# Optimization experiments

Hardware: AMD Instinct MI355X
Metric: run time of the kernel (lower is better)

The kernel has to match this reference:

```python
import jax, jax.numpy as jnp
import numpy as np

B, T, L = 64, 1024, 400
E, D, A, K = 512, 80, 512, 5  # enc_odim, dec_odim, attn_dim, num mixture components


def setup_inputs() -> dict:
    key = jax.random.key(0)
    ks = jax.random.split(key, 24)
    g = lambda k, shape, fan: jax.random.normal(k, shape, jnp.float32) / np.sqrt(fan)
    return {
        "enc_z": jax.random.normal(ks[0], (B, T, E), jnp.float32),
        "ys": jax.random.normal(ks[1], (B, L, D), jnp.float32),
        "pre_W1": g(ks[2], (D, D), D), "pre_b1": jnp.zeros((D,), jnp.float32),
        "pre_W2": g(ks[3], (D, D), D), "pre_b2": jnp.zeros((D,), jnp.float32),
        # MOL attention GRU cell: input D -> hidden A (gates r,z,n)
        "gru_Wx": g(ks[4], (D, 3 * A), D), "gru_Wh": g(ks[5], (A, 3 * A), A),
        "gru_bx": jnp.zeros((3 * A,), jnp.float32), "gru_bh": jnp.zeros((3 * A,), jnp.float32),
        # MOL param net: Linear(A,A) + tanh + Linear(A, 3K)
        "att_W1": g(ks[6], (A, A), A), "att_b1": jnp.zeros((A,), jnp.float32),
        "att_W2": g(ks[7], (A, 3 * K), A), "att_b2": jnp.zeros((3 * K,), jnp.float32),
        # 2-layer LSTM: layer1 input E+A -> D, layer2 D -> D (gates i,f,g,o)
        "lstm_Wx1": g(ks[8], (E + A, 4 * D), E + A), "lstm_Wh1": g(ks[9], (D, 4 * D), D),
        "lstm_b1": jnp.zeros((4 * D,), jnp.float32),
        "lstm_Wx2": g(ks[10], (D, 4 * D), D), "lstm_Wh2": g(ks[11], (D, 4 * D), D),
        "lstm_b2": jnp.zeros((4 * D,), jnp.float32),
        # stop token projection
        "stop_W": g(ks[12], (D, 1), D), "stop_b": jnp.zeros((1,), jnp.float32),
    }


def _gru_cell(x, h, Wx, Wh, bx, bh):
    gx = x @ Wx + bx
    gh = h @ Wh + bh
    xr, xz, xn = jnp.split(gx, 3, axis=-1)
    hr, hz, hn = jnp.split(gh, 3, axis=-1)
    r = jax.nn.sigmoid(xr + hr)
    z = jax.nn.sigmoid(xz + hz)
    n = jnp.tanh(xn + r * hn)
    return (1.0 - z) * n + z * h


def _lstm_cell(x, h, c, Wx, Wh, b):
    gates = x @ Wx + h @ Wh + b
    i, f, g_, o = jnp.split(gates, 4, axis=-1)
    c_new = jax.nn.sigmoid(f) * c + jax.nn.sigmoid(i) * jnp.tanh(g_)
    h_new = jax.nn.sigmoid(o) * jnp.tanh(c_new)
    return h_new, c_new


def reference(enc_z, ys, pre_W1, pre_b1, pre_W2, pre_b2,
              gru_Wx, gru_Wh, gru_bx, gru_bh,
              att_W1, att_b1, att_W2, att_b2,
              lstm_Wx1, lstm_Wh1, lstm_b1, lstm_Wx2, lstm_Wh2, lstm_b2,
              stop_W, stop_b):
    b, t, e = enc_z.shape
    n_steps = ys.shape[1]
    d = pre_W1.shape[0]
    a = gru_Wh.shape[0]
    k = att_W2.shape[1] // 3
    pos = jnp.arange(t, dtype=jnp.float32)  # encoder positions

    def step(carry, _):
        h_att, means, h1, c1, h2, c2, prev_out = carry
        # prenet (eval mode)
        p = jax.nn.relu(prev_out @ pre_W1 + pre_b1)
        p = jax.nn.relu(p @ pre_W2 + pre_b2)
        # MOL attention: update attention RNN state, predict mixture params
        h_att = _gru_cell(p, h_att, gru_Wx, gru_Wh, gru_bx, gru_bh)
        params = jnp.tanh(h_att @ att_W1 + att_b1) @ att_W2 + att_b2  # [B, 3K]
        mu_hat, s_hat, w_hat = jnp.split(params, 3, axis=-1)
        means = means + jax.nn.softplus(mu_hat)            # monotonic means [B, K]
        scales = jax.nn.softplus(s_hat) + 1e-4             # [B, K]
        mix_w = jax.nn.softmax(w_hat, axis=-1)             # [B, K]
        # attention weights via logistic CDF differences: [B, T, K] -> [B, T]
        z_hi = (pos[None, :, None] + 0.5 - means[:, None, :]) / scales[:, None, :]
        z_lo = (pos[None, :, None] - 0.5 - means[:, None, :]) / scales[:, None, :]
        attn_w = jnp.einsum('btk,bk->bt', jax.nn.sigmoid(z_hi) - jax.nn.sigmoid(z_lo), mix_w)
        context = jnp.einsum('bt,bte->be', attn_w, enc_z)  # [B, E]
        # 2-layer LSTM
        x = jnp.concatenate([context, h_att], axis=-1)     # [B, E+A]
        h1, c1 = _lstm_cell(x, h1, c1, lstm_Wx1, lstm_Wh1, lstm_b1)
        h2, c2 = _lstm_cell(h1, h2, c2, lstm_Wx2, lstm_Wh2, lstm_b2)
        logit = (h2 @ stop_W + stop_b)[:, 0]               # [B]
        new_carry = (h_att, means, h1, c1, h2, c2, h2)     # feedback = decoder output
        return new_carry, (h2, logit)

    zf = lambda *s: jnp.zeros(s, jnp.float32)
    carry0 = (zf(b, a), zf(b, k), zf(b, d), zf(b, d), zf(b, d), zf(b, d), zf(b, d))
    _, (outs, logits) = jax.lax.scan(step, carry0, xs=None, length=n_steps)
    before = jnp.transpose(outs, (1, 0, 2))   # [B, L, D]
    after = before                             # postnet not applied inside loop
    return after, before, jnp.transpose(logits, (1, 0))  # [B, L]
```

## Files before the change

### kernel.cpp

```cpp
#include <hip/hip_runtime.h>

#define NB 256
#define BT 512
#define BB 64
#define TT 1024
#define LL 400
#define EE 512
#define DD 80
#define AA 512
#define KK 5

#define WF_HB 2048
#define WF_PP 34816
#define WF_PL 51200
#define WF_EW 112640
#define WF_EWSZ (64UL*1024UL*320UL)

struct Pr {
  const float *enc;
  const float *pW1,*pb1,*pW2,*pb2;
  const float *gWx,*gWh,*gbx,*gbh;
  const float *aW1,*ab1,*aW2,*ab2;
  const float *lWx1,*lWh1,*lb1,*lWx2,*lWh2,*lb2;
  const float *sW,*sb;
  float *oa,*obf,*ol;
  unsigned *ctr;
  float *hb,*pp,*pls,*ew;
  int useEW;
};

__device__ __forceinline__ float sigm(float x){ return 1.f/(1.f+expf(-x)); }
__device__ __forceinline__ float softplusf(float x){ return fmaxf(x,0.f)+log1pf(expf(-fabsf(x))); }
__device__ __forceinline__ void gstore(float* p, float v){
  __hip_atomic_store(p, v, __ATOMIC_RELAXED, __HIP_MEMORY_SCOPE_AGENT);
}
__device__ __forceinline__ float gload(const float* p){
  return __hip_atomic_load(p, __ATOMIC_RELAXED, __HIP_MEMORY_SCOPE_AGENT);
}
__device__ __forceinline__ void gadd(float* p, float v){
  __hip_atomic_fetch_add(p, v, __ATOMIC_RELAXED, __HIP_MEMORY_SCOPE_AGENT);
}
__device__ __forceinline__ void acc4(float4& a, float w, const float4 x){
  a.x = fmaf(w,x.x,a.x); a.y = fmaf(w,x.y,a.y);
  a.z = fmaf(w,x.z,a.z); a.w = fmaf(w,x.w,a.w);
}

__device__ __forceinline__ void cbar_arrive(unsigned* ctr){
  __syncthreads();
  if (threadIdx.x == 0){
    asm volatile("s_waitcnt vmcnt(0)" ::: "memory");
    __hip_atomic_fetch_add(ctr, 1u, __ATOMIC_RELAXED, __HIP_MEMORY_SCOPE_AGENT);
  }
}
__device__ __forceinline__ void cbar_wait(unsigned* ctr, unsigned& tgt){
  if (threadIdx.x == 0){
    while (__hip_atomic_load(ctr, __ATOMIC_RELAXED, __HIP_MEMORY_SCOPE_AGENT) < tgt)
      __builtin_amdgcn_s_sleep(1);
  }
  __syncthreads();
  tgt += 16;
}

__global__ __launch_bounds__(512) void ew_kernel(const float* __restrict__ enc,
                                                 const float* __restrict__ W,
                                                 float* __restrict__ EW){
  const int b = blockIdx.x, t0 = blockIdx.y*16, tid = threadIdx.x;
  __shared__ float encT[512*16];
  #pragma unroll
  for (int r=0;r<16;++r)
    encT[tid*16+r] = enc[((size_t)b*TT + t0 + r)*EE + tid];
  __syncthreads();
  if (tid < 320){
    float acc[16];
    #pragma unroll
    for (int k=0;k<16;++k) acc[k]=0.f;
    const float* wp = W + tid;
    #pragma unroll 2
    for (int e=0;e<512;++e){
      float w = wp[(size_t)e*320];
      const float4* er = (const float4*)&encT[e*16];
      float4 x0=er[0], x1=er[1], x2=er[2], x3=er[3];
      acc[0]=fmaf(w,x0.x,acc[0]); acc[1]=fmaf(w,x0.y,acc[1]);
      acc[2]=fmaf(w,x0.z,acc[2]); acc[3]=fmaf(w,x0.w,acc[3]);
      acc[4]=fmaf(w,x1.x,acc[4]); acc[5]=fmaf(w,x1.y,acc[5]);
      acc[6]=fmaf(w,x1.z,acc[6]); acc[7]=fmaf(w,x1.w,acc[7]);
      acc[8]=fmaf(w,x2.x,acc[8]); acc[9]=fmaf(w,x2.y,acc[9]);
      acc[10]=fmaf(w,x2.z,acc[10]); acc[11]=fmaf(w,x2.w,acc[11]);
      acc[12]=fmaf(w,x3.x,acc[12]); acc[13]=fmaf(w,x3.y,acc[13]);
      acc[14]=fmaf(w,x3.z,acc[14]); acc[15]=fmaf(w,x3.w,acc[15]);
    }
    #pragma unroll
    for (int k=0;k<16;++k)
      EW[((size_t)b*TT + t0 + k)*320 + tid] = acc[k];
  }
}

__global__ __launch_bounds__(BT) void decoder_kernel(Pr P){
  const int blk = blockIdx.x, tid = threadIdx.x;
  const int sq = blk & 15, coh = blk >> 4;
  const int b0 = coh * 4;
  unsigned* ctr = P.ctr + coh*64;

  __shared__ float4 hj4[512];
  __shared__ float4 pj4[DD];
  __shared__ float4 h1j4[DD];
  __shared__ float4 h2j4[DD];
  __shared__ float4 qs4[32];
  __shared__ float4 ctx4[32];
  __shared__ float4 l2a4[320];
  __shared__ float4 scr4[2048];
  __shared__ float  awb[4][1024];
  __shared__ float  c1s[4][80], c2s[4][80];
  __shared__ float  pv[4][16], msta[4][8], mscl[4][8], mwt[4][8];
  __shared__ float  stp[320];
  __shared__ int    wlo[4], whi[4];

  float* hjF=(float*)hj4;  float* pjF=(float*)pj4;  float* h1F=(float*)h1j4;
  float* h2F=(float*)h2j4; float* scrF=(float*)scr4; float* qsF=(float*)qs4;

  { float4 z{};
    for (int i=tid;i<512;i+=BT) hj4[i]=z;
    for (int i=tid;i<1536;i+=BT) scr4[512+i]=z;
    if (tid<DD){ h1j4[tid]=z; h2j4[tid]=z; }
    if (tid<320){ c1s[tid&3][tid>>2]=0.f; c2s[tid&3][tid>>2]=0.f; }
    if (tid<32) msta[tid>>3][tid&7]=0.f;
  }
  if (tid<320){
    #pragma unroll
    for (int par=0;par<3;++par)
      #pragma unroll
      for (int g=0;g<4;++g)
        gstore(&P.pls[par*20480 + (size_t)(b0+g)*320 + tid], 0.f);
  }
  unsigned tgt = 16;
  cbar_arrive(ctr); cbar_wait(ctr, tgt);

  for (int l=0; l<LL; ++l){
    float* plA = P.pls + (l%3)*20480;
    float* plZ = P.pls + ((l+1)%3)*20480;
    const int wr = l & 15;

    if (tid<320){
      const int col=tid>>2, g=tid&3;
      float s=P.pb1[col];
      #pragma unroll 4
      for (int j=0;j<DD;++j) s = fmaf(h2F[j*4+g], P.pW1[j*DD+col], s);
      scrF[col*4+g]=fmaxf(s,0.f);
    }
    __syncthreads();
    if (tid<320){
      const int col=tid>>2, g=tid&3;
      float s=P.pb2[col];
      #pragma unroll 4
      for (int j=0;j<DD;++j) s = fmaf(scrF[j*4+g], P.pW2[j*DD+col], s);
      pjF[col*4+g]=fmaxf(s,0.f);
    }
    __syncthreads();

    if (tid<128){
      const int u = tid & 31, psl = tid >> 5;
      const int cb = sq*32 + u;
      float4 ar{}, az{}, axn{};
      const int j0 = psl*20;
      #pragma unroll 4
      for (int jj=0;jj<20;++jj){
        const int j = j0+jj;
        float4 x = pj4[j];
        const float* W = P.gWx + (size_t)j*1536 + cb;
        acc4(ar,W[0],x); acc4(az,W[512],x); acc4(axn,W[1024],x);
      }
      scr4[0*128 + psl*32+u]=ar;
      scr4[1*128 + psl*32+u]=az;
      scr4[2*128 + psl*32+u]=axn;
    }
    __syncthreads();
    if (tid<128){
      const int u=tid>>2, g=tid&3, uu=sq*32+u;
      float rx=0,zx=0,xn=0,hn=0;
      #pragma unroll
      for (int k=0;k<4;++k){
        rx += scrF[(0*128+k*32+u)*4+g];
        zx += scrF[(1*128+k*32+u)*4+g];
        xn += scrF[(2*128+k*32+u)*4+g];
      }
      #pragma unroll
      for (int k=0;k<16;++k){
        rx += scrF[(512 + 0*512 + k*32+u)*4+g];
        zx += scrF[(512 + 1*512 + k*32+u)*4+g];
        hn += scrF[(512 + 2*512 + k*32+u)*4+g];
      }
      float r = sigm(rx + P.gbx[uu] + P.gbh[uu]);
      float z = sigm(zx + P.gbx[512+uu] + P.gbh[512+uu]);
      float n = tanhf(xn + P.gbx[1024+uu] + r*(hn + P.gbh[1024+uu]));
      float ho = (1.f-z)*n + z*hjF[uu*4+g];
      gstore(&P.hb[(size_t)(b0+g)*512 + uu], ho);
    }
    cbar_arrive(ctr);
    if (tid<320){
      float4 a{};
      const float* W = P.lWh2 + tid;
      #pragma unroll 4
      for (int j=0;j<DD;++j) acc4(a, W[(size_t)j*320], h2j4[j]);
      l2a4[tid]=a;
    }
    cbar_wait(ctr, tgt);
    {
      float4 h;
      h.x=gload(&P.hb[(size_t)(b0+0)*512+tid]);
      h.y=gload(&P.hb[(size_t)(b0+1)*512+tid]);
      h.z=gload(&P.hb[(size_t)(b0+2)*512+tid]);
      h.w=gload(&P.hb[(size_t)(b0+3)*512+tid]);
      hj4[tid]=h;
    }
    __syncthreads();

    {
      const int c = tid & 31, jsl = tid >> 5, j0 = jsl*32;
      float4 a{};
      const float* W = P.aW1 + (size_t)j0*512 + sq*32 + c;
      #pragma unroll 4
      for (int jj=0;jj<32;++jj) acc4(a, W[(size_t)jj*512], hj4[j0+jj]);
      scr4[jsl*32+c]=a;
    }
    __syncthreads();
    if (tid<128){
      const int c=tid>>2, g=tid&3;
      float s=0.f;
      #pragma unroll
      for (int k=0;k<16;++k) s += scrF[(k*32+c)*4+g];
      qsF[c*4+g] = tanhf(s + P.ab1[sq*32+c]);
    }
    __syncthreads();
    if (tid<60){
      const int col=tid%15, g=tid/15;
      float s=0.f;
      #pragma unroll 4
      for (int j=0;j<32;++j) s = fmaf(qsF[j*4+g], P.aW2[(size_t)(sq*32+j)*15+col], s);
      gstore(&P.pp[(size_t)(b0+g)*256 + sq*16 + col], s);
    }
    cbar_arrive(ctr);
    float4 l1acc{};
    if (tid<320){
      { const float* W = P.lWx1 + (size_t)(512+sq*32)*320 + tid;
        #pragma unroll 4
        for (int j=0;j<32;++j) acc4(l1acc, W[(size_t)j*320], hj4[sq*32+j]); }
      { const float* W = P.lWh1 + (size_t)(sq*5)*320 + tid;
        #pragma unroll
        for (int j=0;j<5;++j)  acc4(l1acc, W[(size_t)j*320], h1j4[sq*5+j]); }
    }
    cbar_wait(ctr, tgt);
    if (tid<60){
      const int col=tid%15, g=tid/15;
      float s=P.ab2[col];
      #pragma unroll
      for (int k=0;k<16;++k) s += gload(&P.pp[(size_t)(b0+g)*256 + k*16 + col]);
      pv[g][col]=s;
    }
    __syncthreads();
    if (tid<4){
      const int g=tid;
      float lo=3.4e38f, hi=-3.4e38f, mmax=-3.4e38f;
      #pragma unroll
      for (int k=0;k<KK;++k){
        float m = msta[g][k] + softplusf(pv[g][k]);
        msta[g][k]=m;
        float sc = softplusf(pv[g][5+k]) + 1e-4f;
        mscl[g][k]=sc;
        mmax = fmaxf(mmax, pv[g][10+k]);
        lo = fminf(lo, m-0.5f-16.f*sc);
        hi = fmaxf(hi, m+0.5f+16.f*sc);
      }
      float den=0.f;
      #pragma unroll
      for (int k=0;k<KK;++k){ float e=expf(pv[g][10+k]-mmax); mwt[g][k]=e; den+=e; }
      float rd=1.f/den;
      #pragma unroll
      for (int k=0;k<KK;++k) mwt[g][k]*=rd;
      int ilo=(int)fmaxf(0.f,floorf(lo));
      int ihi=(int)fminf((float)TT,ceilf(hi)+1.f);
      if (ihi<ilo) ihi=ilo;
      wlo[g]=ilo; whi[g]=ihi;
    }
    __syncthreads();

    if (P.useEW){
      { const int g = tid>>7, lane = tid&127;
        const int lo_=wlo[g], hi_=whi[g];
        for (int t = lo_+lane; t < hi_; t += 128){
          const float tf=(float)t;
          float s=0.f;
          #pragma unroll
          for (int k=0;k<KK;++k){
            float mu=msta[g][k], sc=mscl[g][k];
            s += mwt[g][k]*(sigm((tf+0.5f-mu)/sc)-sigm((tf-0.5f-mu)/sc));
          }
          awb[g][t-lo_]=s;
        }
      }
      __syncthreads();
      if (tid<320){
        float* lp=(float*)&l1acc;
        const float* EWb = P.ew;
        #pragma unroll
        for (int g=0;g<4;++g){
          const int lo_=wlo[g], hi_=whi[g];
          for (int t=lo_+sq; t<hi_; t+=16)
            lp[g] = fmaf(awb[g][t-lo_], EWb[((size_t)(b0+g)*TT+t)*320+tid], lp[g]);
        }
      }
    } else {
      { const int eq = tid&7, g = (tid>>3)&3, ts = tid>>5;
        const float* bz = P.enc + (size_t)(b0+g)*TT*EE + sq*32 + eq*4;
        float4 acc{};
        for (int t = wlo[g]+ts; t < whi[g]; t += 16){
          const float tf=(float)t;
          float awv=0.f;
          #pragma unroll
          for (int k=0;k<KK;++k){
            float mu=msta[g][k], sc=mscl[g][k];
            awv += mwt[g][k]*(sigm((tf+0.5f-mu)/sc)-sigm((tf-0.5f-mu)/sc));
          }
          float4 v = *(const float4*)(bz+(size_t)t*EE);
          acc.x=fmaf(awv,v.x,acc.x); acc.y=fmaf(awv,v.y,acc.y);
          acc.z=fmaf(awv,v.z,acc.z); acc.w=fmaf(awv,v.w,acc.w);
        }
        ((float4*)scrF)[ts*32 + g*8 + eq]=acc;
      }
      __syncthreads();
      if (tid<128){
        const int g=tid>>5, e=tid&31;
        float s=0.f;
        #pragma unroll
        for (int k=0;k<16;++k) s += scrF[(k*32 + g*8 + (e>>2))*4 + (e&3)];
        ((float*)&ctx4[e])[g]=s;
      }
      __syncthreads();
      if (tid<320){
        const float* W = P.lWx1 + (size_t)(sq*32)*320 + tid;
        #pragma unroll 4
        for (int j=0;j<32;++j) acc4(l1acc, W[(size_t)j*320], ctx4[j]);
      }
    }
    if (tid<320){
      float* lp=(float*)&l1acc;
      #pragma unroll
      for (int g=0;g<4;++g) gadd(&plA[(size_t)(b0+g)*320 + tid], lp[g]);
    }
    cbar_arrive(ctr);
    {
      const int u = tid & 31, hsl = tid >> 5;
      const int cb = sq*32 + u;
      float4 ar{}, az{}, ahn{};
      const int h0 = hsl*32;
      #pragma unroll 4
      for (int jj=0;jj<32;++jj){
        float4 x = hj4[h0+jj];
        const float* W = P.gWh + (size_t)(h0+jj)*1536 + cb;
        acc4(ar,W[0],x); acc4(az,W[512],x); acc4(ahn,W[1024],x);
      }
      scr4[512 + 0*512 + hsl*32+u]=ar;
      scr4[512 + 1*512 + hsl*32+u]=az;
      scr4[512 + 2*512 + hsl*32+u]=ahn;
    }
    cbar_wait(ctr, tgt);
    if (tid<320){
      const int u=tid>>2, g=tid&3;
      float gate[4];
      #pragma unroll
      for (int gg=0;gg<4;++gg)
        gate[gg] = gload(&plA[(size_t)(b0+g)*320 + gg*80 + u]) + P.lb1[gg*80+u];
      float i_=sigm(gate[0]), f_=sigm(gate[1]), g_=tanhf(gate[2]), o_=sigm(gate[3]);
      float cn=f_*c1s[g][u]+i_*g_;
      c1s[g][u]=cn;
      h1F[u*4+g]=o_*tanhf(cn);
    }
    if (sq==wr && tid<320){
      #pragma unroll
      for (int g=0;g<4;++g) gstore(&plZ[(size_t)(b0+g)*320 + tid], 0.f);
    }
    __syncthreads();
    if (tid<320){
      float4 a = l2a4[tid];
      const float* W = P.lWx2 + tid;
      #pragma unroll 4
      for (int j=0;j<DD;++j) acc4(a, W[(size_t)j*320], h1j4[j]);
      const float bb=P.lb2[tid];
      a.x+=bb; a.y+=bb; a.z+=bb; a.w+=bb;
      scr4[tid]=a;
    }
    __syncthreads();
    if (tid<320){
      const int u=tid>>2, g=tid&3;
      float i_=sigm(scrF[(0*80+u)*4+g]);
      float f_=sigm(scrF[(1*80+u)*4+g]);
      float g_=tanhf(scrF[(2*80+u)*4+g]);
      float o_=sigm(scrF[(3*80+u)*4+g]);
      float cn=f_*c2s[g][u]+i_*g_;
      c2s[g][u]=cn;
      float hn=o_*tanhf(cn);
      h2F[u*4+g]=hn;
      stp[u*4+g]=hn*P.sW[u];
      if (sq==wr){
        const size_t o=((size_t)(b0+g)*LL+l)*DD+u;
        P.oa[o]=hn; P.obf[o]=hn;
      }
    }
    __syncthreads();
    if (tid<4 && sq==wr){
      float s=P.sb[0];
      for (int u=0;u<DD;++u) s+=stp[u*4+tid];
      P.ol[(size_t)(b0+tid)*LL+l]=s;
    }
  }
}

extern "C" void kernel_launch(void* const* d_in, const int* in_sizes, int n_in,
                              void* d_out, int out_size, void* d_ws, size_t ws_size,
                              hipStream_t stream){
  (void)in_sizes; (void)n_in; (void)out_size;
  if (ws_size < (size_t)WF_EW*sizeof(float)) return;
  const int useEW = ws_size >= (size_t)(WF_EW + WF_EWSZ)*sizeof(float);

  hipMemsetAsync(d_ws, 0, 8192, stream);

  Pr P;
  P.enc = (const float*)d_in[0];
  P.pW1=(const float*)d_in[2];  P.pb1=(const float*)d_in[3];
  P.pW2=(const float*)d_in[4];  P.pb2=(const float*)d_in[5];
  P.gWx=(const float*)d_in[6];  P.gWh=(const float*)d_in[7];
  P.gbx=(const float*)d_in[8];  P.gbh=(const float*)d_in[9];
  P.aW1=(const float*)d_in[10]; P.ab1=(const float*)d_in[11];
  P.aW2=(const float*)d_in[12]; P.ab2=(const float*)d_in[13];
  P.lWx1=(const float*)d_in[14]; P.lWh1=(const float*)d_in[15]; P.lb1=(const float*)d_in[16];
  P.lWx2=(const float*)d_in[17]; P.lWh2=(const float*)d_in[18]; P.lb2=(const float*)d_in[19];
  P.sW=(const float*)d_in[20];  P.sb=(const float*)d_in[21];

  float* ws = (float*)d_ws;
  P.ctr = (unsigned*)ws;
  P.hb  = ws + WF_HB;
  P.pp  = ws + WF_PP;
  P.pls = ws + WF_PL;
  P.ew  = ws + WF_EW;
  P.useEW = useEW;

  if (useEW)
    ew_kernel<<<dim3(BB, TT/16), 512, 0, stream>>>(P.enc, P.lWx1, P.ew);

  float* o = (float*)d_out;
  P.oa  = o;
  P.obf = o + (size_t)BB*LL*DD;
  P.ol  = o + (size_t)2*BB*LL*DD;

  void* args[] = { (void*)&P };
  hipLaunchCooperativeKernel((void*)decoder_kernel, dim3(NB), dim3(BT), args, 0, stream);
}
```

Before: 10.86 ms.

## Overlap GRU recurrent matvec with barrier waits and atomically reduce MOL params

The GRU hidden-state matvec is split so its first 12 rows are computed while waiting on the grid barrier after the attention-param phase, and the rest are computed after the next arrive. MOL param partials are now accumulated with atomic adds into a triple-buffered per-step array instead of stored as 16 partial slices and summed after the barrier. Zeroing of the next LSTM partial-sum buffer is spread across all blocks using otherwise idle threads before the arrive, rather than done by one block afterwards. This aims to hide barrier latency and shorten the serial critical path, at the cost of extra atomics and more live registers across the barrier.

```diff
diff --git a/kernel.cpp b/kernel.cpp
--- a/kernel.cpp
+++ b/kernel.cpp
@@ -132,12 +132,19 @@
       for (int g=0;g<4;++g)
         gstore(&P.pls[par*20480 + (size_t)(b0+g)*320 + tid], 0.f);
   }
+  if (tid<64){
+    #pragma unroll
+    for (int par=0;par<3;++par)
+      gstore(&P.pp[par*1024 + (size_t)(b0 + (tid>>4))*16 + (tid&15)], 0.f);
+  }
   unsigned tgt = 16;
   cbar_arrive(ctr); cbar_wait(ctr, tgt);
 
   for (int l=0; l<LL; ++l){
     float* plA = P.pls + (l%3)*20480;
     float* plZ = P.pls + ((l+1)%3)*20480;
+    float* ppA = P.pp  + (l%3)*1024;
+    float* ppZ = P.pp  + ((l+1)%3)*1024;
     const int wr = l & 15;
 
     if (tid<320){
@@ -236,10 +243,13 @@
       float s=0.f;
       #pragma unroll 4
       for (int j=0;j<32;++j) s = fmaf(qsF[j*4+g], P.aW2[(size_t)(sq*32+j)*15+col], s);
-      gstore(&P.pp[(size_t)(b0+g)*256 + sq*16 + col], s);
+      gadd(&ppA[(size_t)(b0+g)*16 + col], s);
     }
     cbar_arrive(ctr);
     float4 l1acc{};
+    float4 g_ar{}, g_az{}, g_ahn{};
+    const int gu = tid & 31, ghsl = tid >> 5;
+    const int gcb = sq*32 + gu, gh0 = ghsl*32;
     if (tid<320){
       { const float* W = P.lWx1 + (size_t)(512+sq*32)*320 + tid;
         #pragma unroll 4
@@ -248,13 +258,18 @@
         #pragma unroll
         for (int j=0;j<5;++j)  acc4(l1acc, W[(size_t)j*320], h1j4[sq*5+j]); }
     }
+    {
+      #pragma unroll 4
+      for (int jj=0;jj<12;++jj){
+        float4 x = hj4[gh0+jj];
+        const float* W = P.gWh + (size_t)(gh0+jj)*1536 + gcb;
+        acc4(g_ar,W[0],x); acc4(g_az,W[512],x); acc4(g_ahn,W[1024],x);
+      }
+    }
     cbar_wait(ctr, tgt);
     if (tid<60){
       const int col=tid%15, g=tid/15;
-      float s=P.ab2[col];
-      #pragma unroll
-      for (int k=0;k<16;++k) s += gload(&P.pp[(size_t)(b0+g)*256 + k*16 + col]);
-      pv[g][col]=s;
+      pv[g][col] = gload(&ppA[(size_t)(b0+g)*16 + col]) + P.ab2[col];
     }
     __syncthreads();
     if (tid<4){
@@ -346,21 +361,25 @@
       #pragma unroll
       for (int g=0;g<4;++g) gadd(&plA[(size_t)(b0+g)*320 + tid], lp[g]);
     }
+    if (tid>=384 && tid<464){
+      const int t2=tid-384, c=sq*20+(t2>>2), g=t2&3;
+      gstore(&plZ[(size_t)(b0+g)*320 + c], 0.f);
+    }
+    if (sq==wr && tid>=320 && tid<380){
+      const int t2=tid-320, col=t2%15, g=t2/15;
+      gstore(&ppZ[(size_t)(b0+g)*16 + col], 0.f);
+    }
     cbar_arrive(ctr);
     {
-      const int u = tid & 31, hsl = tid >> 5;
-      const int cb = sq*32 + u;
-      float4 ar{}, az{}, ahn{};
-      const int h0 = hsl*32;
-      #pragma unroll 4
-      for (int jj=0;jj<32;++jj){
-        float4 x = hj4[h0+jj];
-        const float* W = P.gWh + (size_t)(h0+jj)*1536 + cb;
-        acc4(ar,W[0],x); acc4(az,W[512],x); acc4(ahn,W[1024],x);
-      }
-      scr4[512 + 0*512 + hsl*32+u]=ar;
-      scr4[512 + 1*512 + hsl*32+u]=az;
-      scr4[512 + 2*512 + hsl*32+u]=ahn;
+      #pragma unroll 4
+      for (int jj=12;jj<32;++jj){
+        float4 x = hj4[gh0+jj];
+        const float* W = P.gWh + (size_t)(gh0+jj)*1536 + gcb;
+        acc4(g_ar,W[0],x); acc4(g_az,W[512],x); acc4(g_ahn,W[1024],x);
+      }
+      scr4[512 + 0*512 + ghsl*32+gu]=g_ar;
+      scr4[512 + 1*512 + ghsl*32+gu]=g_az;
+      scr4[512 + 2*512 + ghsl*32+gu]=g_ahn;
     }
     cbar_wait(ctr, tgt);
     if (tid<320){
@@ -373,10 +392,6 @@
       float cn=f_*c1s[g][u]+i_*g_;
       c1s[g][u]=cn;
       h1F[u*4+g]=o_*tanhf(cn);
-    }
-    if (sq==wr && tid<320){
-      #pragma unroll
-      for (int g=0;g<4;++g) gstore(&plZ[(size_t)(b0+g)*320 + tid], 0.f);
     }
     __syncthreads();
     if (tid<320){
```

Measured after the change: 10.89 ms. No clear change (+0.3%).
